# Optimization experiments

Hardware: AMD Instinct MI355X
Metric: run time of the kernel (lower is better)

## Reference

```python
import jax, jax.numpy as jnp
import numpy as np

N_NODES = 10000


def gcn_conv(x, W, b, src, dst, num_nodes):
    """PyG GCNConv: add self-loops, symmetric deg^{-1/2} normalization,
    linear transform (no bias in lin), scatter-add aggregation, then bias."""
    xw = x @ W  # (N, H)
    # degree on A + I (self-loops added)
    deg = jnp.zeros((num_nodes,), dtype=x.dtype).at[dst].add(1.0) + 1.0
    dinv = jax.lax.rsqrt(deg)  # (N,)
    norm = dinv[src] * dinv[dst]  # (E,)
    msg = xw[src] * norm[:, None]  # (E, H) gathered messages
    agg = jax.ops.segment_sum(msg, dst, num_segments=num_nodes)
    # self-loop contribution: norm_ii = dinv_i^2
    agg = agg + xw * (dinv * dinv)[:, None]
    return agg + b


def setup_inputs() -> dict:
    key = jax.random.key(0)
    k1, k2, k3, k4 = jax.random.split(key, 4)
    N, F, H, E = N_NODES, 256, 512, 320000
    x = jax.random.normal(k1, (N, F), dtype=jnp.float32)
    edge_index = jax.random.randint(k2, (2, E), 0, N, dtype=jnp.int64)
    W1 = jax.random.normal(k3, (F, H), dtype=jnp.float32) * (1.0 / np.sqrt(F))
    b1 = jnp.zeros((H,), dtype=jnp.float32)
    W2 = jax.random.normal(k4, (H, F), dtype=jnp.float32) * (1.0 / np.sqrt(H))
    b2 = jnp.zeros((F,), dtype=jnp.float32)
    return {"x": x, "edge_index": edge_index, "W1": W1, "b1": b1, "W2": W2, "b2": b2}


def reference(x, edge_index, W1, b1, W2, b2):
    src, dst = edge_index[0], edge_index[1]
    h = jax.nn.relu(gcn_conv(x, W1, b1, src, dst, N_NODES))
    h = jax.nn.relu(gcn_conv(h, W2, b2, src, dst, N_NODES))
    # global_max_pool with single graph (batch all zeros) -> (1, F)
    return jnp.max(h, axis=0, keepdims=True)
```

## Files before the change

### kernel.cpp

```cpp
#include <hip/hip_runtime.h>

#define NNODES 10000
#define MP 10112
#define F 256
#define H 512
#define CAP 128
#define H1STR 520
#define ZROW NNODES

typedef _Float16 half8 __attribute__((ext_vector_type(8)));
typedef float floatx4 __attribute__((ext_vector_type(4)));
typedef float floatx8 __attribute__((ext_vector_type(8)));

__global__ __launch_bounds__(256) void zero_k(int* __restrict__ cnt) {
  int gt = blockIdx.x * 256 + threadIdx.x;
  if (gt < NNODES) cnt[gt] = 0;
}

__global__ __launch_bounds__(256) void build_k(const int* __restrict__ src,
                                               const int* __restrict__ dst,
                                               int* __restrict__ cnt,
                                               int* __restrict__ csr, int E) {
  int e = blockIdx.x * blockDim.x + threadIdx.x;
  if (e < E) {
    int d = dst[e];
    int p = atomicAdd(&cnt[d], 1);
    if (p < CAP) csr[(size_t)d * CAP + p] = src[e];
  }
}

__global__ __launch_bounds__(256) void prep_k(const float* __restrict__ W1,
                                              const float* __restrict__ W2,
                                              const float* __restrict__ x,
                                              const int* __restrict__ cnt,
                                              _Float16* __restrict__ W1t,
                                              _Float16* __restrict__ W2t,
                                              _Float16* __restrict__ xh,
                                              float* __restrict__ dinv) {
  int gt = blockIdx.x * 256 + threadIdx.x;
  if (gt < NNODES) dinv[gt] = rsqrtf((float)(cnt[gt] + 1));
  if (gt < H * F) {
    W1t[gt] = (_Float16)W1[(gt & 255) * H + (gt >> 8)];
    W2t[gt] = (_Float16)W2[(gt & 511) * F + (gt >> 9)];
  }
  if (gt < NNODES * F / 8) {
    int row = gt >> 5;
    float di = rsqrtf((float)(cnt[row] + 1));
    floatx8 v = *(const floatx8*)(x + (size_t)gt * 8);
    #pragma unroll
    for (int t = 0; t < 8; t++) v[t] *= di;
    *(half8*)(xh + (size_t)gt * 8) = __builtin_convertvector(v, half8);
  }
  if (gt < F / 8) {
    half8 z = {};
    *(half8*)(xh + (size_t)ZROW * F + (size_t)gt * 8) = z;
  }
}

template <bool FUSE_MAX>
__global__ __launch_bounds__(256) void aggb_k(const _Float16* __restrict__ in,
                                              const int* __restrict__ cnt,
                                              const int* __restrict__ csr,
                                              const float* __restrict__ bias,
                                              _Float16* __restrict__ outh,
                                              float* __restrict__ out) {
  __shared__ float smem[2048];
  int tid = threadIdx.x;
  int lane = tid & 63, wvi = tid >> 6;
  int half = lane >> 5, hl = lane & 31;
  int f0 = hl * 8;
  int node = (blockIdx.x * 4 + wvi) * 2 + half;
  float one = 1.0f;
  asm("" : "+v"(one));
  floatx8 bb = {};
  if (FUSE_MAX) bb = *(const floatx8*)(bias + f0);

  int degfull = cnt[node];
  int deg = min(degfull, CAP);
  float di = rsqrtf((float)(degfull + 1));
  const int* bucket = csr + (size_t)node * CAP;
  const _Float16* inf = in + f0;

  half8 xsv = *(const half8*)(inf + (size_t)node * F);
  int sv = ZROW;
  if (hl < deg) sv = bucket[hl];

  floatx8 acc;
  #pragma unroll
  for (int t = 0; t < 8; t++) acc[t] = (float)xsv[t];

  for (int c = 0; c < deg; c += 32) {
    int mm = min(32, deg - c);
    int svn = ZROW;
    int rem = deg - c - 32;
    if (hl < rem) svn = bucket[c + 32 + hl];
    #pragma unroll
    for (int b = 0; b < 2; b++) {
      int base = b * 16;
      if (base < mm) {
        int sj[16];
        #pragma unroll
        for (int u = 0; u < 16; u++) sj[u] = __shfl(sv, (half << 5) | (base + u), 64);
        half8 hv[16];
        #pragma unroll
        for (int u = 0; u < 16; u++)
          hv[u] = *(const half8*)(inf + (size_t)sj[u] * F);
        #pragma unroll
        for (int u = 0; u < 16; u++)
          #pragma unroll
          for (int t = 0; t < 8; t++)
            acc[t] = __builtin_fmaf((float)hv[u][t], one, acc[t]);
      }
    }
    sv = svn;
  }

  if (FUSE_MAX) {
    floatx8 lmax;
    #pragma unroll
    for (int t = 0; t < 8; t++) lmax[t] = fmaxf(di * acc[t] + bb[t], 0.f);
    float* srow = smem + (size_t)(wvi * 2 + half) * 256;
    *(floatx8*)(srow + f0) = lmax;
    __syncthreads();
    float m = smem[tid];
    #pragma unroll
    for (int r = 1; r < 8; r++) m = fmaxf(m, smem[r * 256 + tid]);
    atomicMax((int*)&out[tid], __float_as_int(m));
  } else {
    floatx8 tot;
    #pragma unroll
    for (int t = 0; t < 8; t++) tot[t] = di * acc[t];
    *(half8*)(outh + (size_t)node * F + f0) = __builtin_convertvector(tot, half8);
  }
}

__global__ __launch_bounds__(256) void gemm12_k(const _Float16* __restrict__ A,
                                                const _Float16* __restrict__ W1t,
                                                const float* __restrict__ b1,
                                                const _Float16* __restrict__ W2t,
                                                const float* __restrict__ dinv,
                                                _Float16* __restrict__ C) {
  __shared__ _Float16 h1[32 * H1STR];
  int lane = threadIdx.x & 63;
  int wv = threadIdx.x >> 6;
  int r = lane & 15, q = lane >> 4;
  int m0 = blockIdx.x * 32;

  {
    floatx4 acc[2][8] = {};
    const _Float16* Ap = A + (size_t)(m0 + r) * F + q * 8;
    const _Float16* Bp = W1t + (size_t)(wv * 128 + r) * F + q * 8;
    for (int k0 = 0; k0 < F; k0 += 32) {
      half8 a[2], b[8];
      #pragma unroll
      for (int i = 0; i < 2; i++) a[i] = *(const half8*)(Ap + (size_t)i * 16 * F + k0);
      #pragma unroll
      for (int j = 0; j < 8; j++) b[j] = *(const half8*)(Bp + (size_t)j * 16 * F + k0);
      #pragma unroll
      for (int i = 0; i < 2; i++)
        #pragma unroll
        for (int j = 0; j < 8; j++)
          acc[i][j] = __builtin_amdgcn_mfma_f32_16x16x32_f16(a[i], b[j], acc[i][j], 0, 0, 0);
    }
    #pragma unroll
    for (int i = 0; i < 2; i++) {
      #pragma unroll
      for (int j = 0; j < 8; j++) {
        int n = wv * 128 + j * 16 + r;
        float bv = b1[n];
        #pragma unroll
        for (int rr = 0; rr < 4; rr++) {
          int row = i * 16 + q * 4 + rr;
          h1[row * H1STR + n] = (_Float16)fmaxf(acc[i][j][rr] + bv, 0.f);
        }
      }
    }
  }
  __syncthreads();

  {
    float sc[2][4];
    #pragma unroll
    for (int i = 0; i < 2; i++)
      #pragma unroll
      for (int rr = 0; rr < 4; rr++) {
        int row = m0 + i * 16 + q * 4 + rr;
        sc[i][rr] = (row < NNODES) ? dinv[row] : 0.f;
      }
    floatx4 acc[2][4] = {};
    const _Float16* Bp = W2t + (size_t)(wv * 64 + r) * H + q * 8;
    for (int k0 = 0; k0 < H; k0 += 32) {
      half8 a[2], b[4];
      #pragma unroll
      for (int i = 0; i < 2; i++)
        a[i] = *(const half8*)(h1 + (i * 16 + r) * H1STR + k0 + q * 8);
      #pragma unroll
      for (int j = 0; j < 4; j++) b[j] = *(const half8*)(Bp + (size_t)j * 16 * H + k0);
      #pragma unroll
      for (int i = 0; i < 2; i++)
        #pragma unroll
        for (int j = 0; j < 4; j++)
          acc[i][j] = __builtin_amdgcn_mfma_f32_16x16x32_f16(a[i], b[j], acc[i][j], 0, 0, 0);
    }
    #pragma unroll
    for (int i = 0; i < 2; i++) {
      #pragma unroll
      for (int j = 0; j < 4; j++) {
        int n = wv * 64 + j * 16 + r;
        #pragma unroll
        for (int rr = 0; rr < 4; rr++) {
          int row = m0 + i * 16 + q * 4 + rr;
          float val = (row < NNODES) ? acc[i][j][rr] * sc[i][rr] : 0.f;
          C[(size_t)row * F + n] = (_Float16)val;
        }
      }
    }
  }
}

extern "C" void kernel_launch(void* const* d_in, const int* in_sizes, int n_in,
                              void* d_out, int out_size, void* d_ws, size_t ws_size,
                              hipStream_t stream) {
  const float* x  = (const float*)d_in[0];
  const int*   ei = (const int*)d_in[1];
  const float* W1 = (const float*)d_in[2];
  const float* b1 = (const float*)d_in[3];
  const float* W2 = (const float*)d_in[4];
  const float* b2 = (const float*)d_in[5];
  const int E = in_sizes[1] / 2;
  const int N = NNODES;
  const int* src = ei;
  const int* dst = ei + E;

  char* w = (char*)d_ws;
  size_t off = 0;
  auto take = [&](size_t bytes) -> void* {
    void* p = w + off;
    off += (bytes + 255) & ~(size_t)255;
    return p;
  };
  int*       cnt    = (int*)take((size_t)N * 4);
  int*       csr    = (int*)take((size_t)N * CAP * 4);
  _Float16*  W1t    = (_Float16*)take((size_t)H * F * 2);
  _Float16*  W2t    = (_Float16*)take((size_t)F * H * 2);
  _Float16*  xh     = (_Float16*)take((size_t)(N + 1) * F * 2);
  float*     dinvp  = (float*)take((size_t)N * 4);
  _Float16*  axh    = (_Float16*)take((size_t)MP * F * 2);
  _Float16*  xw2h   = (_Float16*)take((size_t)MP * F * 2);

  zero_k<<<(N + 255) / 256, 256, 0, stream>>>(cnt);
  build_k<<<(E + 255) / 256, 256, 0, stream>>>(src, dst, cnt, csr, E);
  prep_k<<<1250, 256, 0, stream>>>(W1, W2, x, cnt, W1t, W2t, xh, dinvp);
  aggb_k<false><<<1250, 256, 0, stream>>>(xh, cnt, csr, nullptr, axh, nullptr);
  gemm12_k<<<MP / 32, 256, 0, stream>>>(axh, W1t, b1, W2t, dinvp, xw2h);
  aggb_k<true><<<1250, 256, 0, stream>>>(xw2h, cnt, csr, b2, nullptr, (float*)d_out);
}
```

Measured before the change: 180.4 us.

## Fuse first-layer aggregation into GEMM kernel and remap aggregation to one wave per node

The first neighbour aggregation now runs inside the GEMM kernel. Each block gathers its 32 rows into shared memory, which removes the intermediate aggregated buffer and one kernel launch. The aggregation mapping changes from half-wave per node with 8-wide loads to one wave per node with 4-wide loads. The zero-row padding is replaced by clamped indices and a 0/1 mask. The weight transpose moves into the CSR build kernel, and the zeroing kernel becomes a memset. The risk is that the gather in the fused kernel runs on only 316 blocks with 8 sequential nodes per wave, which may expose gather latency.

```diff
diff --git a/kernel.cpp b/kernel.cpp
--- a/kernel.cpp
+++ b/kernel.cpp
@@ -6,154 +6,129 @@
 #define H 512
 #define CAP 128
 #define H1STR 520
-#define ZROW NNODES
-
+#define ASTR 264
+
+typedef _Float16 half4 __attribute__((ext_vector_type(4)));
 typedef _Float16 half8 __attribute__((ext_vector_type(8)));
 typedef float floatx4 __attribute__((ext_vector_type(4)));
 typedef float floatx8 __attribute__((ext_vector_type(8)));
 
-__global__ __launch_bounds__(256) void zero_k(int* __restrict__ cnt) {
-  int gt = blockIdx.x * 256 + threadIdx.x;
-  if (gt < NNODES) cnt[gt] = 0;
-}
-
 __global__ __launch_bounds__(256) void build_k(const int* __restrict__ src,
                                                const int* __restrict__ dst,
                                                int* __restrict__ cnt,
-                                               int* __restrict__ csr, int E) {
-  int e = blockIdx.x * blockDim.x + threadIdx.x;
-  if (e < E) {
-    int d = dst[e];
+                                               int* __restrict__ csr,
+                                               const float* __restrict__ W1,
+                                               const float* __restrict__ W2,
+                                               _Float16* __restrict__ W1t,
+                                               _Float16* __restrict__ W2t, int E) {
+  int gt = blockIdx.x * 256 + threadIdx.x;
+  if (gt < E) {
+    int d = dst[gt];
     int p = atomicAdd(&cnt[d], 1);
-    if (p < CAP) csr[(size_t)d * CAP + p] = src[e];
-  }
-}
-
-__global__ __launch_bounds__(256) void prep_k(const float* __restrict__ W1,
-                                              const float* __restrict__ W2,
-                                              const float* __restrict__ x,
+    if (p < CAP) csr[(size_t)d * CAP + p] = src[gt];
+  }
+  if (gt < H * F) {
+    W1t[gt] = (_Float16)W1[(gt & 255) * H + (gt >> 8)];
+    W2t[gt] = (_Float16)W2[(gt & 511) * F + (gt >> 9)];
+  }
+}
+
+__global__ __launch_bounds__(256) void prep_k(const float* __restrict__ x,
                                               const int* __restrict__ cnt,
-                                              _Float16* __restrict__ W1t,
-                                              _Float16* __restrict__ W2t,
                                               _Float16* __restrict__ xh,
                                               float* __restrict__ dinv) {
   int gt = blockIdx.x * 256 + threadIdx.x;
   if (gt < NNODES) dinv[gt] = rsqrtf((float)(cnt[gt] + 1));
-  if (gt < H * F) {
-    W1t[gt] = (_Float16)W1[(gt & 255) * H + (gt >> 8)];
-    W2t[gt] = (_Float16)W2[(gt & 511) * F + (gt >> 9)];
-  }
   if (gt < NNODES * F / 8) {
     int row = gt >> 5;
     float di = rsqrtf((float)(cnt[row] + 1));
     floatx8 v = *(const floatx8*)(x + (size_t)gt * 8);
     #pragma unroll
     for (int t = 0; t < 8; t++) v[t] *= di;
-    *(half8*)(xh + (size_t)gt * 8) = __builtin_convertvector(v, half8);
-  }
-  if (gt < F / 8) {
-    half8 z = {};
-    *(half8*)(xh + (size_t)ZROW * F + (size_t)gt * 8) = z;
-  }
-}
-
-template <bool FUSE_MAX>
-__global__ __launch_bounds__(256) void aggb_k(const _Float16* __restrict__ in,
-                                              const int* __restrict__ cnt,
-                                              const int* __restrict__ csr,
-                                              const float* __restrict__ bias,
-                                              _Float16* __restrict__ outh,
-                                              float* __restrict__ out) {
-  __shared__ float smem[2048];
-  int tid = threadIdx.x;
-  int lane = tid & 63, wvi = tid >> 6;
-  int half = lane >> 5, hl = lane & 31;
-  int f0 = hl * 8;
-  int node = (blockIdx.x * 4 + wvi) * 2 + half;
-  float one = 1.0f;
-  asm("" : "+v"(one));
-  floatx8 bb = {};
-  if (FUSE_MAX) bb = *(const floatx8*)(bias + f0);
-
-  int degfull = cnt[node];
-  int deg = min(degfull, CAP);
-  float di = rsqrtf((float)(degfull + 1));
+    half8 h = __builtin_convertvector(v, half8);
+    *(half8*)(xh + (size_t)gt * 8) = h;
+  }
+}
+
+__device__ __forceinline__ floatx4 agg_node(const _Float16* __restrict__ in,
+                                            const int* __restrict__ cnt,
+                                            const int* __restrict__ csr,
+                                            int node, int f0, float* dio) {
+  int degf = cnt[node];
+  int deg = min(degf, CAP);
+  *dio = rsqrtf((float)(degf + 1));
   const int* bucket = csr + (size_t)node * CAP;
-  const _Float16* inf = in + f0;
-
-  half8 xsv = *(const half8*)(inf + (size_t)node * F);
-  int sv = ZROW;
-  if (hl < deg) sv = bucket[hl];
-
-  floatx8 acc;
+  half4 sv = *(const half4*)(in + (size_t)node * F + f0);
+  floatx4 acc;
   #pragma unroll
-  for (int t = 0; t < 8; t++) acc[t] = (float)xsv[t];
-
-  for (int c = 0; c < deg; c += 32) {
-    int mm = min(32, deg - c);
-    int svn = ZROW;
-    int rem = deg - c - 32;
-    if (hl < rem) svn = bucket[c + 32 + hl];
-    #pragma unroll
-    for (int b = 0; b < 2; b++) {
-      int base = b * 16;
-      if (base < mm) {
-        int sj[16];
-        #pragma unroll
-        for (int u = 0; u < 16; u++) sj[u] = __shfl(sv, (half << 5) | (base + u), 64);
-        half8 hv[16];
-        #pragma unroll
-        for (int u = 0; u < 16; u++)
-          hv[u] = *(const half8*)(inf + (size_t)sj[u] * F);
-        #pragma unroll
-        for (int u = 0; u < 16; u++)
-          #pragma unroll
-          for (int t = 0; t < 8; t++)
-            acc[t] = __builtin_fmaf((float)hv[u][t], one, acc[t]);
-      }
-    }
-    sv = svn;
-  }
-
-  if (FUSE_MAX) {
-    floatx8 lmax;
-    #pragma unroll
-    for (int t = 0; t < 8; t++) lmax[t] = fmaxf(di * acc[t] + bb[t], 0.f);
-    float* srow = smem + (size_t)(wvi * 2 + half) * 256;
-    *(floatx8*)(srow + f0) = lmax;
-    __syncthreads();
-    float m = smem[tid];
-    #pragma unroll
-    for (int r = 1; r < 8; r++) m = fmaxf(m, smem[r * 256 + tid]);
-    atomicMax((int*)&out[tid], __float_as_int(m));
-  } else {
-    floatx8 tot;
-    #pragma unroll
-    for (int t = 0; t < 8; t++) tot[t] = di * acc[t];
-    *(half8*)(outh + (size_t)node * F + f0) = __builtin_convertvector(tot, half8);
-  }
-}
-
-__global__ __launch_bounds__(256) void gemm12_k(const _Float16* __restrict__ A,
+  for (int t = 0; t < 4; t++) acc[t] = (float)sv[t];
+  int nch = (deg + 15) >> 4;
+  for (int c = 0; c < nch; ++c) {
+    int base = c << 4;
+    const _Float16* rp[16];
+    float mk[16];
+    #pragma unroll
+    for (int u = 0; u < 16; ++u) {
+      int e = base + u;
+      int ce = (e < deg) ? e : (deg - 1);
+      rp[u] = in + (size_t)bucket[ce] * F;
+      mk[u] = (e < deg) ? 1.0f : 0.0f;
+      asm("" : "+v"(mk[u]));
+    }
+    half4 hv[16];
+    #pragma unroll
+    for (int u = 0; u < 16; ++u) hv[u] = *(const half4*)(rp[u] + f0);
+    #pragma unroll
+    for (int u = 0; u < 16; ++u)
+      #pragma unroll
+      for (int t = 0; t < 4; ++t)
+        acc[t] = __builtin_fmaf((float)hv[u][t], mk[u], acc[t]);
+  }
+  return acc;
+}
+
+__global__ __launch_bounds__(256) void aggemm_k(const _Float16* __restrict__ xh,
+                                                const int* __restrict__ cnt,
+                                                const int* __restrict__ csr,
                                                 const _Float16* __restrict__ W1t,
                                                 const float* __restrict__ b1,
                                                 const _Float16* __restrict__ W2t,
                                                 const float* __restrict__ dinv,
                                                 _Float16* __restrict__ C) {
+  __shared__ _Float16 Asm[32 * ASTR];
   __shared__ _Float16 h1[32 * H1STR];
-  int lane = threadIdx.x & 63;
-  int wv = threadIdx.x >> 6;
+  int tid = threadIdx.x;
+  int lane = tid & 63, wv = tid >> 6;
+  int m0 = blockIdx.x * 32;
+
+  {
+    int f0 = lane * 4;
+    for (int i = 0; i < 8; ++i) {
+      int nl = wv * 8 + i;
+      int node = __builtin_amdgcn_readfirstlane(m0 + nl);
+      half4 o = {};
+      if (node < NNODES) {
+        float di;
+        floatx4 acc = agg_node(xh, cnt, csr, node, f0, &di);
+        floatx4 tot;
+        #pragma unroll
+        for (int t = 0; t < 4; t++) tot[t] = di * acc[t];
+        o = __builtin_convertvector(tot, half4);
+      }
+      *(half4*)(&Asm[nl * ASTR + f0]) = o;
+    }
+  }
+  __syncthreads();
+
   int r = lane & 15, q = lane >> 4;
-  int m0 = blockIdx.x * 32;
-
   {
     floatx4 acc[2][8] = {};
-    const _Float16* Ap = A + (size_t)(m0 + r) * F + q * 8;
     const _Float16* Bp = W1t + (size_t)(wv * 128 + r) * F + q * 8;
     for (int k0 = 0; k0 < F; k0 += 32) {
       half8 a[2], b[8];
       #pragma unroll
-      for (int i = 0; i < 2; i++) a[i] = *(const half8*)(Ap + (size_t)i * 16 * F + k0);
+      for (int i = 0; i < 2; i++)
+        a[i] = *(const half8*)(&Asm[(i * 16 + r) * ASTR + k0 + q * 8]);
       #pragma unroll
       for (int j = 0; j < 8; j++) b[j] = *(const half8*)(Bp + (size_t)j * 16 * F + k0);
       #pragma unroll
@@ -216,6 +191,30 @@
       }
     }
   }
+}
+
+__global__ __launch_bounds__(256) void agg2_k(const _Float16* __restrict__ in,
+                                              const int* __restrict__ cnt,
+                                              const int* __restrict__ csr,
+                                              const float* __restrict__ b2,
+                                              float* __restrict__ out) {
+  __shared__ float smem[1024];
+  int tid = threadIdx.x;
+  int lane = tid & 63, wv = tid >> 6;
+  int f0 = lane * 4;
+  int node = __builtin_amdgcn_readfirstlane(blockIdx.x * 4 + wv);
+  float di;
+  floatx4 acc = agg_node(in, cnt, csr, node, f0, &di);
+  floatx4 bb = *(const floatx4*)(b2 + f0);
+  floatx4 lm;
+  #pragma unroll
+  for (int t = 0; t < 4; t++) lm[t] = fmaxf(di * acc[t] + bb[t], 0.f);
+  *(floatx4*)(smem + wv * 256 + f0) = lm;
+  __syncthreads();
+  float m = smem[tid];
+  #pragma unroll
+  for (int rr = 1; rr < 4; rr++) m = fmaxf(m, smem[rr * 256 + tid]);
+  atomicMax((int*)&out[tid], __float_as_int(m));
 }
 
 extern "C" void kernel_launch(void* const* d_in, const int* in_sizes, int n_in,
@@ -243,15 +242,13 @@
   int*       csr    = (int*)take((size_t)N * CAP * 4);
   _Float16*  W1t    = (_Float16*)take((size_t)H * F * 2);
   _Float16*  W2t    = (_Float16*)take((size_t)F * H * 2);
-  _Float16*  xh     = (_Float16*)take((size_t)(N + 1) * F * 2);
+  _Float16*  xh     = (_Float16*)take((size_t)N * F * 2);
   float*     dinvp  = (float*)take((size_t)N * 4);
-  _Float16*  axh    = (_Float16*)take((size_t)MP * F * 2);
   _Float16*  xw2h   = (_Float16*)take((size_t)MP * F * 2);
 
-  zero_k<<<(N + 255) / 256, 256, 0, stream>>>(cnt);
-  build_k<<<(E + 255) / 256, 256, 0, stream>>>(src, dst, cnt, csr, E);
-  prep_k<<<1250, 256, 0, stream>>>(W1, W2, x, cnt, W1t, W2t, xh, dinvp);
-  aggb_k<false><<<1250, 256, 0, stream>>>(xh, cnt, csr, nullptr, axh, nullptr);
-  gemm12_k<<<MP / 32, 256, 0, stream>>>(axh, W1t, b1, W2t, dinvp, xw2h);
-  aggb_k<true><<<1250, 256, 0, stream>>>(xw2h, cnt, csr, b2, nullptr, (float*)d_out);
-}
+  hipMemsetAsync(cnt, 0, (size_t)N * 4, stream);
+  build_k<<<1250, 256, 0, stream>>>(src, dst, cnt, csr, W1, W2, W1t, W2t, E);
+  prep_k<<<1250, 256, 0, stream>>>(x, cnt, xh, dinvp);
+  aggemm_k<<<MP / 32, 256, 0, stream>>>(xh, cnt, csr, W1t, b1, W2t, dinvp, xw2h);
+  agg2_k<<<2500, 256, 0, stream>>>(xw2h, cnt, csr, b2, (float*)d_out);
+}
```

Measured after the change: 214.6 us. 1.19x slower.

## Stage neighbor byte offsets in LDS for gather and fold weight transpose into build

Applied to the files above, without the earlier changes.

The aggregation kernel now loads each node's full CSR bucket once with vector loads, turns the indices into byte offsets (shift by 9), pads to a multiple of 16 with the zero row, and stores them in shared memory. The gather loop then reads offsets from LDS in place of using cross-lane shuffles, and drops the per-chunk prefetch and bounds logic. Separately, the weight transpose moves from prep_k into build_k, and zero_k is replaced by hipMemsetAsync. Costs: more LDS per block, and every node reads the full 128-entry bucket row regardless of its degree.

```diff
diff --git a/kernel.cpp b/kernel.cpp
--- a/kernel.cpp
+++ b/kernel.cpp
@@ -11,38 +11,34 @@
 typedef _Float16 half8 __attribute__((ext_vector_type(8)));
 typedef float floatx4 __attribute__((ext_vector_type(4)));
 typedef float floatx8 __attribute__((ext_vector_type(8)));
-
-__global__ __launch_bounds__(256) void zero_k(int* __restrict__ cnt) {
-  int gt = blockIdx.x * 256 + threadIdx.x;
-  if (gt < NNODES) cnt[gt] = 0;
-}
+typedef int intx4 __attribute__((ext_vector_type(4)));
 
 __global__ __launch_bounds__(256) void build_k(const int* __restrict__ src,
                                                const int* __restrict__ dst,
                                                int* __restrict__ cnt,
-                                               int* __restrict__ csr, int E) {
-  int e = blockIdx.x * blockDim.x + threadIdx.x;
-  if (e < E) {
-    int d = dst[e];
+                                               int* __restrict__ csr,
+                                               const float* __restrict__ W1,
+                                               const float* __restrict__ W2,
+                                               _Float16* __restrict__ W1t,
+                                               _Float16* __restrict__ W2t, int E) {
+  int gt = blockIdx.x * 256 + threadIdx.x;
+  if (gt < E) {
+    int d = dst[gt];
     int p = atomicAdd(&cnt[d], 1);
-    if (p < CAP) csr[(size_t)d * CAP + p] = src[e];
-  }
-}
-
-__global__ __launch_bounds__(256) void prep_k(const float* __restrict__ W1,
-                                              const float* __restrict__ W2,
-                                              const float* __restrict__ x,
+    if (p < CAP) csr[(size_t)d * CAP + p] = src[gt];
+  }
+  if (gt < H * F) {
+    W1t[gt] = (_Float16)W1[(gt & 255) * H + (gt >> 8)];
+    W2t[gt] = (_Float16)W2[(gt & 511) * F + (gt >> 9)];
+  }
+}
+
+__global__ __launch_bounds__(256) void prep_k(const float* __restrict__ x,
                                               const int* __restrict__ cnt,
-                                              _Float16* __restrict__ W1t,
-                                              _Float16* __restrict__ W2t,
                                               _Float16* __restrict__ xh,
                                               float* __restrict__ dinv) {
   int gt = blockIdx.x * 256 + threadIdx.x;
   if (gt < NNODES) dinv[gt] = rsqrtf((float)(cnt[gt] + 1));
-  if (gt < H * F) {
-    W1t[gt] = (_Float16)W1[(gt & 255) * H + (gt >> 8)];
-    W2t[gt] = (_Float16)W2[(gt & 511) * F + (gt >> 9)];
-  }
   if (gt < NNODES * F / 8) {
     int row = gt >> 5;
     float di = rsqrtf((float)(cnt[row] + 1));
@@ -64,63 +60,60 @@
                                               const float* __restrict__ bias,
                                               _Float16* __restrict__ outh,
                                               float* __restrict__ out) {
+  __shared__ int buck[8 * CAP];
   __shared__ float smem[2048];
   int tid = threadIdx.x;
   int lane = tid & 63, wvi = tid >> 6;
   int half = lane >> 5, hl = lane & 31;
   int f0 = hl * 8;
+  int lanebyte = hl * 16;
+  int hw = wvi * 2 + half;
   int node = (blockIdx.x * 4 + wvi) * 2 + half;
+  int* lb = buck + hw * CAP;
   float one = 1.0f;
   asm("" : "+v"(one));
   floatx8 bb = {};
   if (FUSE_MAX) bb = *(const floatx8*)(bias + f0);
 
-  int degfull = cnt[node];
-  int deg = min(degfull, CAP);
-  float di = rsqrtf((float)(degfull + 1));
-  const int* bucket = csr + (size_t)node * CAP;
-  const _Float16* inf = in + f0;
-
-  half8 xsv = *(const half8*)(inf + (size_t)node * F);
-  int sv = ZROW;
-  if (hl < deg) sv = bucket[hl];
-
+  int degf = cnt[node];
+  int deg = min(degf, CAP);
+  float di = rsqrtf((float)(degf + 1));
+
+  intx4 bv = *(const intx4*)(csr + (size_t)node * CAP + hl * 4);
+  #pragma unroll
+  for (int j = 0; j < 4; j++) bv[j] <<= 9;
+  *(intx4*)(lb + hl * 4) = bv;
+  int degp = (deg + 15) & ~15;
+  if (hl < degp - deg) lb[deg + hl] = ZROW << 9;
+
+  const char* inb = (const char*)in;
+  half8 xsv = *(const half8*)(in + (size_t)node * F + f0);
   floatx8 acc;
   #pragma unroll
   for (int t = 0; t < 8; t++) acc[t] = (float)xsv[t];
 
-  for (int c = 0; c < deg; c += 32) {
-    int mm = min(32, deg - c);
-    int svn = ZROW;
-    int rem = deg - c - 32;
-    if (hl < rem) svn = bucket[c + 32 + hl];
-    #pragma unroll
-    for (int b = 0; b < 2; b++) {
-      int base = b * 16;
-      if (base < mm) {
-        int sj[16];
-        #pragma unroll
-        for (int u = 0; u < 16; u++) sj[u] = __shfl(sv, (half << 5) | (base + u), 64);
-        half8 hv[16];
-        #pragma unroll
-        for (int u = 0; u < 16; u++)
-          hv[u] = *(const half8*)(inf + (size_t)sj[u] * F);
-        #pragma unroll
-        for (int u = 0; u < 16; u++)
-          #pragma unroll
-          for (int t = 0; t < 8; t++)
-            acc[t] = __builtin_fmaf((float)hv[u][t], one, acc[t]);
-      }
-    }
-    sv = svn;
+  for (int c = 0; c < degp; c += 16) {
+    intx4 iv[4];
+    #pragma unroll
+    for (int j = 0; j < 4; j++) iv[j] = *(const intx4*)(lb + c + j * 4);
+    half8 hv[16];
+    #pragma unroll
+    for (int j = 0; j < 4; j++)
+      #pragma unroll
+      for (int k = 0; k < 4; k++)
+        hv[j * 4 + k] = *(const half8*)(inb + (iv[j][k] + lanebyte));
+    #pragma unroll
+    for (int u = 0; u < 16; u++)
+      #pragma unroll
+      for (int t = 0; t < 8; t++)
+        acc[t] = __builtin_fmaf((float)hv[u][t], one, acc[t]);
   }
 
   if (FUSE_MAX) {
-    floatx8 lmax;
-    #pragma unroll
-    for (int t = 0; t < 8; t++) lmax[t] = fmaxf(di * acc[t] + bb[t], 0.f);
-    float* srow = smem + (size_t)(wvi * 2 + half) * 256;
-    *(floatx8*)(srow + f0) = lmax;
+    floatx8 lm;
+    #pragma unroll
+    for (int t = 0; t < 8; t++) lm[t] = fmaxf(di * acc[t] + bb[t], 0.f);
+    *(floatx8*)(smem + hw * 256 + f0) = lm;
     __syncthreads();
     float m = smem[tid];
     #pragma unroll
@@ -248,9 +241,9 @@
   _Float16*  axh    = (_Float16*)take((size_t)MP * F * 2);
   _Float16*  xw2h   = (_Float16*)take((size_t)MP * F * 2);
 
-  zero_k<<<(N + 255) / 256, 256, 0, stream>>>(cnt);
-  build_k<<<(E + 255) / 256, 256, 0, stream>>>(src, dst, cnt, csr, E);
-  prep_k<<<1250, 256, 0, stream>>>(W1, W2, x, cnt, W1t, W2t, xh, dinvp);
+  hipMemsetAsync(cnt, 0, (size_t)N * 4, stream);
+  build_k<<<1250, 256, 0, stream>>>(src, dst, cnt, csr, W1, W2, W1t, W2t, E);
+  prep_k<<<1250, 256, 0, stream>>>(x, cnt, xh, dinvp);
   aggb_k<false><<<1250, 256, 0, stream>>>(xh, cnt, csr, nullptr, axh, nullptr);
   gemm12_k<<<MP / 32, 256, 0, stream>>>(axh, W1t, b1, W2t, dinvp, xw2h);
   aggb_k<true><<<1250, 256, 0, stream>>>(xw2h, cnt, csr, b2, nullptr, (float*)d_out);
```

Result: faster. 175.2 us (-2.9%).
